# Optimization experiments

Measured on AMD Instinct MI355X. Metric: run time of the kernel, lower is better.

## Reference

```python
import jax, jax.numpy as jnp
import numpy as np

N = 100000   # num nodes
E = 640000   # num edges
IN, H, OUT = 6, 128, 1
BN_EPS = 1e-5


def setup_inputs() -> dict:
    key = jax.random.key(0)
    ks = jax.random.split(key, 12)
    x = jax.random.normal(ks[0], (N, IN), dtype=jnp.float32)
    edge_index = jax.random.randint(ks[1], (2, E), 0, N, dtype=jnp.int64)
    def lin(k, fin, fout):
        s = 1.0 / np.sqrt(fin)
        return jax.random.uniform(k, (fin, fout), jnp.float32, -s, s)
    return {
        "x": x,
        "edge_index": edge_index,
        "W1": lin(ks[2], IN, H),  "b1": jnp.zeros((H,), jnp.float32),
        "W2": lin(ks[3], H, H),   "b2": jnp.zeros((H,), jnp.float32),
        "W3": lin(ks[4], H, OUT), "b3": jnp.zeros((OUT,), jnp.float32),
        "g1": jnp.ones((H,), jnp.float32),  "be1": jnp.zeros((H,), jnp.float32),
        "g2": jnp.ones((H,), jnp.float32),  "be2": jnp.zeros((H,), jnp.float32),
    }


def _gcn_norm(edge_index):
    # add self-loops, then symmetric normalization D^-1/2 (A+I) D^-1/2
    loop = jnp.arange(N, dtype=edge_index.dtype)
    src = jnp.concatenate([edge_index[0], loop])
    dst = jnp.concatenate([edge_index[1], loop])
    deg = jax.ops.segment_sum(jnp.ones_like(dst, dtype=jnp.float32), dst, num_segments=N)
    dis = jnp.where(deg > 0, jax.lax.rsqrt(deg), 0.0)
    norm = dis[src] * dis[dst]  # (E+N,)
    return src, dst, norm


def _conv(h, W, b, src, dst, norm):
    m = h @ W                                   # (N, out) linear transform first
    msg = m[src] * norm[:, None]                # gather + edge scaling
    return jax.ops.segment_sum(msg, dst, num_segments=N) + b


def _bn(h, g, be):
    mu = h.mean(axis=0)
    var = h.var(axis=0)  # biased, as torch BN uses for normalization
    return g * (h - mu) * jax.lax.rsqrt(var + BN_EPS) + be


def reference(x, edge_index, W1, b1, W2, b2, W3, b3, g1, be1, g2, be2):
    src, dst, norm = _gcn_norm(edge_index)
    h = jax.nn.relu(_bn(_conv(x, W1, b1, src, dst, norm), g1, be1))
    h = jax.nn.relu(_bn(_conv(h, W2, b2, src, dst, norm), g2, be2))
    out = _conv(h, W3, b3, src, dst, norm)
    return jax.nn.sigmoid(out)  # (N, 1) risk scores
```

## Files before the change

### kernel.cpp

```cpp
#include <hip/hip_runtime.h>
#include <hip/hip_bf16.h>
#include <math.h>

#define HDIM 128
#define BN_EPS 1e-5f
#define CHUNK 512
#define TM 64

__device__ __forceinline__ int eget(const void* ei, long long pos, int is64) {
    return is64 ? (int)((const long long*)ei)[pos] : ((const int*)ei)[pos];
}

__global__ void k_detect(const int* ei32, int* flag) {
    if (threadIdx.x == 0) {
        int nz = 0;
        for (int k = 0; k < 64; ++k) nz += (ei32[2 * k + 1] != 0);
        *flag = (nz < 8) ? 1 : 0;
    }
}

__global__ void k_count(const void* ei, const int* flag, int* cnt, int E) {
    int e = blockIdx.x * blockDim.x + threadIdx.x;
    if (e < E) {
        int d = eget(ei, (long long)E + e, *flag);
        atomicAdd(&cnt[d], 1);
    }
}

__global__ void k_dis(const int* cnt, float* dis, int N) {
    int i = blockIdx.x * blockDim.x + threadIdx.x;
    if (i < N) dis[i] = rsqrtf((float)(cnt[i] + 1));
}

__global__ void k_scan1(const int* cnt, int* bsum, int N) {
    __shared__ int s[256];
    int t = threadIdx.x;
    int i = blockIdx.x * CHUNK + t;
    int v = 0;
    if (i < N) v += cnt[i];
    if (i + 256 < N && t + 256 < CHUNK) v += cnt[i + 256];
    s[t] = v; __syncthreads();
    for (int o = 128; o > 0; o >>= 1) {
        if (t < o) s[t] += s[t + o];
        __syncthreads();
    }
    if (t == 0) bsum[blockIdx.x] = s[0];
}

__global__ void k_scan2(int* bsum, int nb) {
    __shared__ int s[512];
    int t = threadIdx.x;
    int carry = 0;
    for (int base = 0; base < nb; base += 512) {
        int i = base + t;
        int v = (i < nb) ? bsum[i] : 0;
        s[t] = v; __syncthreads();
        for (int o = 1; o < 512; o <<= 1) {
            int add = (t >= o) ? s[t - o] : 0;
            __syncthreads();
            s[t] += add;
            __syncthreads();
        }
        if (i < nb) bsum[i] = carry + s[t] - v;
        carry += s[511];
        __syncthreads();
    }
}

__global__ void k_scan3(const int* cnt, const int* bsum, int* rowptr, int N) {
    __shared__ int s[CHUNK];
    int t = threadIdx.x;
    int i = blockIdx.x * CHUNK + t;
    int v = (i < N) ? cnt[i] : 0;
    s[t] = v; __syncthreads();
    for (int o = 1; o < CHUNK; o <<= 1) {
        int add = (t >= o) ? s[t - o] : 0;
        __syncthreads();
        s[t] += add;
        __syncthreads();
    }
    if (i < N) rowptr[i] = bsum[blockIdx.x] + s[t] - v;
    if (i == N - 1) rowptr[N] = bsum[blockIdx.x] + s[t];
}

__global__ void k_fillcsr(const void* ei, const int* flag, const float* dis,
                          const int* rowptr, int* fill, int* esrc, float* enorm, int E) {
    int e = blockIdx.x * blockDim.x + threadIdx.x;
    if (e < E) {
        int is64 = *flag;
        int s = eget(ei, e, is64);
        int d = eget(ei, (long long)E + e, is64);
        int pos = rowptr[d] + atomicAdd(&fill[d], 1);
        esrc[pos] = s;
        enorm[pos] = dis[s] * dis[d];
    }
}

__global__ void k_gath_x(const float* __restrict__ x, const int* __restrict__ rowptr,
                         const int* __restrict__ esrc, const float* __restrict__ enorm,
                         const float* __restrict__ dis, float* __restrict__ aggx, int N) {
    int i = blockIdx.x * blockDim.x + threadIdx.x;
    if (i < N) {
        float d = dis[i], d2 = d * d;
        float a0 = x[i * 6 + 0] * d2, a1 = x[i * 6 + 1] * d2, a2 = x[i * 6 + 2] * d2;
        float a3 = x[i * 6 + 3] * d2, a4 = x[i * 6 + 4] * d2, a5 = x[i * 6 + 5] * d2;
        int p0 = rowptr[i], p1 = rowptr[i + 1];
        for (int p = p0; p < p1; ++p) {
            int s = esrc[p];
            float nr = enorm[p];
            a0 += x[s * 6 + 0] * nr; a1 += x[s * 6 + 1] * nr; a2 += x[s * 6 + 2] * nr;
            a3 += x[s * 6 + 3] * nr; a4 += x[s * 6 + 4] * nr; a5 += x[s * 6 + 5] * nr;
        }
        aggx[i * 6 + 0] = a0; aggx[i * 6 + 1] = a1; aggx[i * 6 + 2] = a2;
        aggx[i * 6 + 3] = a3; aggx[i * 6 + 4] = a4; aggx[i * 6 + 5] = a5;
    }
}

__global__ void k_gemm6(const float* __restrict__ aggx, const float* __restrict__ W1,
                        const float* __restrict__ b1, float* __restrict__ out,
                        float* __restrict__ S, int N) {
    __shared__ float w[6 * HDIM];
    __shared__ float bb[HDIM];
    __shared__ float sh1[256], sh2[256];
    for (int t = threadIdx.x; t < 6 * HDIM; t += blockDim.x) w[t] = W1[t];
    if (threadIdx.x < HDIM) bb[threadIdx.x] = b1[threadIdx.x];
    __syncthreads();
    int j = threadIdx.x & (HDIM - 1);
    int sub = threadIdx.x >> 7;
    float s1 = 0.f, s2 = 0.f;
    for (long long i = blockIdx.x * 2 + sub; i < N; i += (long long)gridDim.x * 2) {
        const float* r = &aggx[i * 6];
        float acc = bb[j];
        acc += r[0] * w[0 * HDIM + j];
        acc += r[1] * w[1 * HDIM + j];
        acc += r[2] * w[2 * HDIM + j];
        acc += r[3] * w[3 * HDIM + j];
        acc += r[4] * w[4 * HDIM + j];
        acc += r[5] * w[5 * HDIM + j];
        out[i * HDIM + j] = acc;
        s1 += acc; s2 += acc * acc;
    }
    sh1[threadIdx.x] = s1; sh2[threadIdx.x] = s2;
    __syncthreads();
    if (threadIdx.x < HDIM) {
        atomicAdd(&S[j], sh1[j] + sh1[j + HDIM]);
        atomicAdd(&S[HDIM + j], sh2[j] + sh2[j + HDIM]);
    }
}

__global__ void k_bnparams(const float* S, const float* g, const float* be,
                           float invN, float* P) {
    int j = threadIdx.x;
    if (j < HDIM) {
        float mu = S[j] * invN;
        float var = S[HDIM + j] * invN - mu * mu;
        float a = g[j] * rsqrtf(var + BN_EPS);
        P[j] = a;
        P[HDIM + j] = be[j] - mu * a;
    }
}

__global__ __launch_bounds__(512, 4)
void k_agg_gemm(const float* __restrict__ h1,
                const float* __restrict__ P1,
                const int* __restrict__ rowptr, const int* __restrict__ esrc,
                const float* __restrict__ enorm, const float* __restrict__ dis,
                const float* __restrict__ W, const float* __restrict__ b,
                float* __restrict__ out,
                float* __restrict__ S,
                int N) {
    __shared__ float At[TM * HDIM];
    const int tid = threadIdx.x;
    const long long i0 = (long long)blockIdx.x * TM;

    {
        const int l = tid & 31;
        const int q = tid >> 5;
        const int c4 = l * 4;
        const float4 pa = *(const float4*)&P1[c4];
        const float4 pb = *(const float4*)&P1[HDIM + c4];
        for (int nn = q; nn < TM; nn += 16) {
            long long i = i0 + nn;
            float4 acc = make_float4(0.f, 0.f, 0.f, 0.f);
            if (i < N) {
                float d = dis[i], d2 = d * d;
                float4 v = *(const float4*)&h1[i * HDIM + c4];
                acc.x = fmaxf(fmaf(pa.x, v.x, pb.x), 0.f) * d2;
                acc.y = fmaxf(fmaf(pa.y, v.y, pb.y), 0.f) * d2;
                acc.z = fmaxf(fmaf(pa.z, v.z, pb.z), 0.f) * d2;
                acc.w = fmaxf(fmaf(pa.w, v.w, pb.w), 0.f) * d2;
                int p0 = rowptr[i], p1e = rowptr[i + 1];
                for (int p = p0; p < p1e; ++p) {
                    int s = esrc[p];
                    float nr = enorm[p];
                    float4 u = *(const float4*)&h1[(long long)s * HDIM + c4];
                    acc.x += fmaxf(fmaf(pa.x, u.x, pb.x), 0.f) * nr;
                    acc.y += fmaxf(fmaf(pa.y, u.y, pb.y), 0.f) * nr;
                    acc.z += fmaxf(fmaf(pa.z, u.z, pb.z), 0.f) * nr;
                    acc.w += fmaxf(fmaf(pa.w, u.w, pb.w), 0.f) * nr;
                }
            }
            *(float4*)&At[nn * HDIM + c4] = acc;
        }
    }
    __syncthreads();

    const int cg = tid & 31;
    const int rg = tid >> 5;
    const int c0 = cg * 4;
    const int r0 = rg * 4;
    float acc[4][4];
    {
        const float4 bv = *(const float4*)&b[c0];
        #pragma unroll
        for (int rr = 0; rr < 4; ++rr) {
            acc[rr][0] = bv.x; acc[rr][1] = bv.y; acc[rr][2] = bv.z; acc[rr][3] = bv.w;
        }
    }
    for (int k = 0; k < HDIM; k += 4) {
        const float4 w0 = *(const float4*)&W[(k + 0) * HDIM + c0];
        const float4 w1 = *(const float4*)&W[(k + 1) * HDIM + c0];
        const float4 w2 = *(const float4*)&W[(k + 2) * HDIM + c0];
        const float4 w3 = *(const float4*)&W[(k + 3) * HDIM + c0];
        #pragma unroll
        for (int rr = 0; rr < 4; ++rr) {
            const float4 av = *(const float4*)&At[(r0 + rr) * HDIM + k];
            acc[rr][0] = fmaf(av.x, w0.x, acc[rr][0]);
            acc[rr][1] = fmaf(av.x, w0.y, acc[rr][1]);
            acc[rr][2] = fmaf(av.x, w0.z, acc[rr][2]);
            acc[rr][3] = fmaf(av.x, w0.w, acc[rr][3]);
            acc[rr][0] = fmaf(av.y, w1.x, acc[rr][0]);
            acc[rr][1] = fmaf(av.y, w1.y, acc[rr][1]);
            acc[rr][2] = fmaf(av.y, w1.z, acc[rr][2]);
            acc[rr][3] = fmaf(av.y, w1.w, acc[rr][3]);
            acc[rr][0] = fmaf(av.z, w2.x, acc[rr][0]);
            acc[rr][1] = fmaf(av.z, w2.y, acc[rr][1]);
            acc[rr][2] = fmaf(av.z, w2.z, acc[rr][2]);
            acc[rr][3] = fmaf(av.z, w2.w, acc[rr][3]);
            acc[rr][0] = fmaf(av.w, w3.x, acc[rr][0]);
            acc[rr][1] = fmaf(av.w, w3.y, acc[rr][1]);
            acc[rr][2] = fmaf(av.w, w3.z, acc[rr][2]);
            acc[rr][3] = fmaf(av.w, w3.w, acc[rr][3]);
        }
    }

    float cs1[4] = {0.f, 0.f, 0.f, 0.f};
    float cs2[4] = {0.f, 0.f, 0.f, 0.f};
    #pragma unroll
    for (int rr = 0; rr < 4; ++rr) {
        long long i = i0 + r0 + rr;
        if (i < N) {
            float4 o = make_float4(acc[rr][0], acc[rr][1], acc[rr][2], acc[rr][3]);
            *(float4*)&out[i * HDIM + c0] = o;
            #pragma unroll
            for (int cc = 0; cc < 4; ++cc) {
                float v = acc[rr][cc];
                cs1[cc] += v; cs2[cc] += v * v;
            }
        }
    }

    __syncthreads();
    #pragma unroll
    for (int cc = 0; cc < 4; ++cc) {
        At[rg * HDIM + c0 + cc]        = cs1[cc];
        At[2048 + rg * HDIM + c0 + cc] = cs2[cc];
    }
    __syncthreads();
    if (tid < 256) {
        int j = tid & (HDIM - 1);
        int which = tid >> 7;
        const float* bp = &At[which * 2048 + j];
        float s = 0.f;
        #pragma unroll
        for (int g = 0; g < 16; ++g) s += bp[g * HDIM];
        atomicAdd(&S[which * HDIM + j], s);
    }
}

__global__ void k_gemv2(const float* __restrict__ A, const float* __restrict__ P,
                        const float* __restrict__ W3, float* __restrict__ m3, int N) {
    int l = threadIdx.x & 31;
    int row = blockIdx.x * 8 + (threadIdx.x >> 5);
    if (row < N) {
        int c4 = l * 4;
        float4 pa = *(const float4*)&P[c4];
        float4 pb = *(const float4*)&P[HDIM + c4];
        float4 w  = *(const float4*)&W3[c4];
        float4 v  = *(const float4*)&A[(long long)row * HDIM + c4];
        float s = fmaxf(fmaf(pa.x, v.x, pb.x), 0.f) * w.x
                + fmaxf(fmaf(pa.y, v.y, pb.y), 0.f) * w.y
                + fmaxf(fmaf(pa.z, v.z, pb.z), 0.f) * w.z
                + fmaxf(fmaf(pa.w, v.w, pb.w), 0.f) * w.w;
        for (int o = 16; o > 0; o >>= 1) s += __shfl_down(s, o, 32);
        if (l == 0) m3[row] = s;
    }
}

__global__ void k_gath_o(const float* __restrict__ m3, const int* __restrict__ rowptr,
                         const int* __restrict__ esrc, const float* __restrict__ enorm,
                         const float* __restrict__ dis, const float* __restrict__ b3,
                         float* __restrict__ out, int N) {
    int i = blockIdx.x * blockDim.x + threadIdx.x;
    if (i < N) {
        float d = dis[i];
        float acc = m3[i] * d * d;
        int p0 = rowptr[i], p1 = rowptr[i + 1];
        for (int p = p0; p < p1; ++p)
            acc += m3[esrc[p]] * enorm[p];
        acc += b3[0];
        out[i] = 1.f / (1.f + expf(-acc));
    }
}

extern "C" void kernel_launch(void* const* d_in, const int* in_sizes, int n_in,
                              void* d_out, int out_size, void* d_ws, size_t ws_size,
                              hipStream_t stream) {
    const float* x  = (const float*)d_in[0];
    const void*  ei = d_in[1];
    const float* W1 = (const float*)d_in[2];
    const float* b1 = (const float*)d_in[3];
    const float* W2 = (const float*)d_in[4];
    const float* b2 = (const float*)d_in[5];
    const float* W3 = (const float*)d_in[6];
    const float* b3 = (const float*)d_in[7];
    const float* g1 = (const float*)d_in[8];
    const float* be1 = (const float*)d_in[9];
    const float* g2 = (const float*)d_in[10];
    const float* be2 = (const float*)d_in[11];

    const int N = in_sizes[0] / 6;
    const int E = in_sizes[1] / 2;
    const float invN = 1.0f / (float)N;

    float* ws = (float*)d_ws;
    long long off = 0;
    int*   flag   = (int*)ws;                 off += 16;
    float* dis    = ws + off;                 off += N;
    int*   cnt    = (int*)(ws + off);         off += N;
    int*   rowptr = (int*)(ws + off);         off += N + 16;
    int*   esrc   = (int*)(ws + off);         off += E;
    float* enorm  = ws + off;                 off += E;
    int*   bsum   = (int*)(ws + off);         off += 512;
    float* S1     = ws + off;                 off += 256;
    float* S2     = ws + off;                 off += 256;
    float* P1     = ws + off;                 off += 256;
    float* P2     = ws + off;                 off += 256;
    float* aggx   = ws + off;                 off += (long long)6 * N;
    float* m3     = ws + off;                 off += N;
    float* Hb1    = ws + off;                 off += (long long)HDIM * N;
    float* Hb2    = ws + off;                 off += (long long)HDIM * N;

    const int T = 256;
    const int bN  = (N + T - 1) / T;
    const int bE  = (E + T - 1) / T;
    const int nchunk = (N + CHUNK - 1) / CHUNK;
    const int ntile  = (N + TM - 1) / TM;

    hipMemsetAsync(S1, 0, 512 * sizeof(float), stream);
    k_detect<<<1, 64, 0, stream>>>((const int*)ei, flag);
    hipMemsetAsync(cnt, 0, (size_t)N * sizeof(int), stream);
    k_count<<<bE, T, 0, stream>>>(ei, flag, cnt, E);
    k_dis<<<bN, T, 0, stream>>>(cnt, dis, N);
    k_scan1<<<nchunk, 256, 0, stream>>>(cnt, bsum, N);
    k_scan2<<<1, 512, 0, stream>>>(bsum, nchunk);
    k_scan3<<<nchunk, CHUNK, 0, stream>>>(cnt, bsum, rowptr, N);
    hipMemsetAsync(cnt, 0, (size_t)N * sizeof(int), stream);
    k_fillcsr<<<bE, T, 0, stream>>>(ei, flag, dis, rowptr, cnt, esrc, enorm, E);

    k_gath_x<<<bN, T, 0, stream>>>(x, rowptr, esrc, enorm, dis, aggx, N);
    k_gemm6<<<512, T, 0, stream>>>(aggx, W1, b1, Hb1, S1, N);
    k_bnparams<<<1, 128, 0, stream>>>(S1, g1, be1, invN, P1);

    k_agg_gemm<<<ntile, 512, 0, stream>>>(Hb1, P1, rowptr, esrc, enorm, dis,
                                          W2, b2, Hb2, S2, N);
    k_bnparams<<<1, 128, 0, stream>>>(S2, g2, be2, invN, P2);

    k_gemv2<<<(N + 7) / 8, T, 0, stream>>>(Hb2, P2, W3, m3, N);
    k_gath_o<<<bN, T, 0, stream>>>(m3, rowptr, esrc, enorm, dis, b3, (float*)d_out, N);
}
```

Measured before the change: 294.3 us.

## Store layer-1 hidden in bf16, persistent ticket-scheduled agg-gemm, vectorized gathers

Layer-1 hidden activations are written as bf16, halving the bytes moved by the dominant 128-wide neighbor gather in k_agg_gemm. That kernel becomes a persistent grid that pulls tiles from an atomic ticket counter. It gains 8-wide lanes, 4-way unrolled edge loops and a padded LDS stride. The input features are also padded to 8 floats for vector loads, and the final scalar gather is unrolled. These cut gather bandwidth and latency, at the cost of bf16 rounding error in the layer-1 activations and an extra padding kernel.

```diff
diff --git a/kernel.cpp b/kernel.cpp
--- a/kernel.cpp
+++ b/kernel.cpp
@@ -6,9 +6,15 @@
 #define BN_EPS 1e-5f
 #define CHUNK 512
 #define TM 64
+#define LDA 132
 
 __device__ __forceinline__ int eget(const void* ei, long long pos, int is64) {
     return is64 ? (int)((const long long*)ei)[pos] : ((const int*)ei)[pos];
+}
+__device__ __forceinline__ unsigned short f2bf(float f) {
+    unsigned int u = __float_as_uint(f);
+    u += 0x7fffu + ((u >> 16) & 1u);
+    return (unsigned short)(u >> 16);
 }
 
 __global__ void k_detect(const int* ei32, int* flag) {
@@ -96,28 +102,49 @@
     }
 }
 
-__global__ void k_gath_x(const float* __restrict__ x, const int* __restrict__ rowptr,
+__global__ void k_padx(const float* __restrict__ x, float* __restrict__ xp, int N) {
+    int t = blockIdx.x * blockDim.x + threadIdx.x;
+    if (t < N * 8) {
+        int i = t >> 3, c = t & 7;
+        xp[t] = (c < 6) ? x[i * 6 + c] : 0.f;
+    }
+}
+
+__global__ void k_gath_x(const float* __restrict__ xp, const int* __restrict__ rowptr,
                          const int* __restrict__ esrc, const float* __restrict__ enorm,
                          const float* __restrict__ dis, float* __restrict__ aggx, int N) {
     int i = blockIdx.x * blockDim.x + threadIdx.x;
-    if (i < N) {
-        float d = dis[i], d2 = d * d;
-        float a0 = x[i * 6 + 0] * d2, a1 = x[i * 6 + 1] * d2, a2 = x[i * 6 + 2] * d2;
-        float a3 = x[i * 6 + 3] * d2, a4 = x[i * 6 + 4] * d2, a5 = x[i * 6 + 5] * d2;
-        int p0 = rowptr[i], p1 = rowptr[i + 1];
-        for (int p = p0; p < p1; ++p) {
-            int s = esrc[p];
-            float nr = enorm[p];
-            a0 += x[s * 6 + 0] * nr; a1 += x[s * 6 + 1] * nr; a2 += x[s * 6 + 2] * nr;
-            a3 += x[s * 6 + 3] * nr; a4 += x[s * 6 + 4] * nr; a5 += x[s * 6 + 5] * nr;
-        }
-        aggx[i * 6 + 0] = a0; aggx[i * 6 + 1] = a1; aggx[i * 6 + 2] = a2;
-        aggx[i * 6 + 3] = a3; aggx[i * 6 + 4] = a4; aggx[i * 6 + 5] = a5;
-    }
+    if (i >= N) return;
+    float d = dis[i], d2 = d * d;
+    float4 A = *(const float4*)&xp[i * 8];
+    float2 B = *(const float2*)&xp[i * 8 + 4];
+    float a0 = A.x * d2, a1 = A.y * d2, a2 = A.z * d2;
+    float a3 = A.w * d2, a4 = B.x * d2, a5 = B.y * d2;
+    int p = rowptr[i], pe = rowptr[i + 1];
+    for (; p + 2 <= pe; p += 2) {
+        int s0 = esrc[p], s1 = esrc[p + 1];
+        float n0 = enorm[p], n1 = enorm[p + 1];
+        float4 A0 = *(const float4*)&xp[s0 * 8];
+        float2 B0 = *(const float2*)&xp[s0 * 8 + 4];
+        float4 A1 = *(const float4*)&xp[s1 * 8];
+        float2 B1 = *(const float2*)&xp[s1 * 8 + 4];
+        a0 += A0.x * n0 + A1.x * n1; a1 += A0.y * n0 + A1.y * n1;
+        a2 += A0.z * n0 + A1.z * n1; a3 += A0.w * n0 + A1.w * n1;
+        a4 += B0.x * n0 + B1.x * n1; a5 += B0.y * n0 + B1.y * n1;
+    }
+    if (p < pe) {
+        int s0 = esrc[p]; float n0 = enorm[p];
+        float4 A0 = *(const float4*)&xp[s0 * 8];
+        float2 B0 = *(const float2*)&xp[s0 * 8 + 4];
+        a0 += A0.x * n0; a1 += A0.y * n0; a2 += A0.z * n0;
+        a3 += A0.w * n0; a4 += B0.x * n0; a5 += B0.y * n0;
+    }
+    aggx[i * 6 + 0] = a0; aggx[i * 6 + 1] = a1; aggx[i * 6 + 2] = a2;
+    aggx[i * 6 + 3] = a3; aggx[i * 6 + 4] = a4; aggx[i * 6 + 5] = a5;
 }
 
 __global__ void k_gemm6(const float* __restrict__ aggx, const float* __restrict__ W1,
-                        const float* __restrict__ b1, float* __restrict__ out,
+                        const float* __restrict__ b1, unsigned short* __restrict__ out,
                         float* __restrict__ S, int N) {
     __shared__ float w[6 * HDIM];
     __shared__ float bb[HDIM];
@@ -137,7 +164,7 @@
         acc += r[3] * w[3 * HDIM + j];
         acc += r[4] * w[4 * HDIM + j];
         acc += r[5] * w[5 * HDIM + j];
-        out[i * HDIM + j] = acc;
+        out[i * HDIM + j] = f2bf(acc);
         s1 += acc; s2 += acc * acc;
     }
     sh1[threadIdx.x] = s1; sh2[threadIdx.x] = s2;
@@ -160,121 +187,157 @@
     }
 }
 
-__global__ __launch_bounds__(512, 4)
-void k_agg_gemm(const float* __restrict__ h1,
-                const float* __restrict__ P1,
+__device__ __forceinline__ void gacc(float* a, const float* pa, const float* pb,
+                                     uint4 u, float wgt) {
+    unsigned int uu[4] = {u.x, u.y, u.z, u.w};
+    #pragma unroll
+    for (int q = 0; q < 4; ++q) {
+        float lo = __uint_as_float(uu[q] << 16);
+        float hi = __uint_as_float(uu[q] & 0xffff0000u);
+        a[2 * q]     += fmaxf(fmaf(pa[2 * q],     lo, pb[2 * q]),     0.f) * wgt;
+        a[2 * q + 1] += fmaxf(fmaf(pa[2 * q + 1], hi, pb[2 * q + 1]), 0.f) * wgt;
+    }
+}
+
+__global__ __launch_bounds__(512, 8)
+void k_agg_gemm(const unsigned short* __restrict__ m1, const float* __restrict__ P1,
                 const int* __restrict__ rowptr, const int* __restrict__ esrc,
                 const float* __restrict__ enorm, const float* __restrict__ dis,
                 const float* __restrict__ W, const float* __restrict__ b,
-                float* __restrict__ out,
-                float* __restrict__ S,
-                int N) {
-    __shared__ float At[TM * HDIM];
+                float* __restrict__ out, float* __restrict__ S,
+                int* __restrict__ ticket, int ntiles, int N) {
+    __shared__ float At[TM * LDA];
+    __shared__ int s_tile;
     const int tid = threadIdx.x;
-    const long long i0 = (long long)blockIdx.x * TM;
-
+
+    const int gl = tid & 15;
+    const int gg = tid >> 4;
+    const int c8 = gl * 8;
+    float pa[8], pb[8];
     {
-        const int l = tid & 31;
-        const int q = tid >> 5;
-        const int c4 = l * 4;
-        const float4 pa = *(const float4*)&P1[c4];
-        const float4 pb = *(const float4*)&P1[HDIM + c4];
-        for (int nn = q; nn < TM; nn += 16) {
-            long long i = i0 + nn;
-            float4 acc = make_float4(0.f, 0.f, 0.f, 0.f);
-            if (i < N) {
-                float d = dis[i], d2 = d * d;
-                float4 v = *(const float4*)&h1[i * HDIM + c4];
-                acc.x = fmaxf(fmaf(pa.x, v.x, pb.x), 0.f) * d2;
-                acc.y = fmaxf(fmaf(pa.y, v.y, pb.y), 0.f) * d2;
-                acc.z = fmaxf(fmaf(pa.z, v.z, pb.z), 0.f) * d2;
-                acc.w = fmaxf(fmaf(pa.w, v.w, pb.w), 0.f) * d2;
-                int p0 = rowptr[i], p1e = rowptr[i + 1];
-                for (int p = p0; p < p1e; ++p) {
-                    int s = esrc[p];
-                    float nr = enorm[p];
-                    float4 u = *(const float4*)&h1[(long long)s * HDIM + c4];
-                    acc.x += fmaxf(fmaf(pa.x, u.x, pb.x), 0.f) * nr;
-                    acc.y += fmaxf(fmaf(pa.y, u.y, pb.y), 0.f) * nr;
-                    acc.z += fmaxf(fmaf(pa.z, u.z, pb.z), 0.f) * nr;
-                    acc.w += fmaxf(fmaf(pa.w, u.w, pb.w), 0.f) * nr;
-                }
-            }
-            *(float4*)&At[nn * HDIM + c4] = acc;
-        }
-    }
-    __syncthreads();
-
+        float4 t0 = *(const float4*)&P1[c8];
+        float4 t1 = *(const float4*)&P1[c8 + 4];
+        float4 t2 = *(const float4*)&P1[HDIM + c8];
+        float4 t3 = *(const float4*)&P1[HDIM + c8 + 4];
+        pa[0] = t0.x; pa[1] = t0.y; pa[2] = t0.z; pa[3] = t0.w;
+        pa[4] = t1.x; pa[5] = t1.y; pa[6] = t1.z; pa[7] = t1.w;
+        pb[0] = t2.x; pb[1] = t2.y; pb[2] = t2.z; pb[3] = t2.w;
+        pb[4] = t3.x; pb[5] = t3.y; pb[6] = t3.z; pb[7] = t3.w;
+    }
     const int cg = tid & 31;
     const int rg = tid >> 5;
     const int c0 = cg * 4;
     const int r0 = rg * 4;
-    float acc[4][4];
-    {
-        const float4 bv = *(const float4*)&b[c0];
+    const float4 bv = *(const float4*)&b[c0];
+
+    for (;;) {
+        if (tid == 0) s_tile = atomicAdd(ticket, 1);
+        __syncthreads();
+        const int tile = s_tile;
+        if (tile >= ntiles) return;
+        const long long i0 = (long long)tile * TM;
+
+        for (int nn = gg; nn < TM; nn += 32) {
+            long long i = i0 + nn;
+            float a[8] = {0.f, 0.f, 0.f, 0.f, 0.f, 0.f, 0.f, 0.f};
+            if (i < N) {
+                float d = dis[i];
+                uint4 us = *(const uint4*)&m1[i * HDIM + c8];
+                gacc(a, pa, pb, us, d * d);
+                int p = rowptr[i], pe = rowptr[i + 1];
+                for (; p + 4 <= pe; p += 4) {
+                    int s0 = esrc[p], s1 = esrc[p + 1], s2 = esrc[p + 2], s3 = esrc[p + 3];
+                    float n0 = enorm[p], n1 = enorm[p + 1], n2 = enorm[p + 2], n3 = enorm[p + 3];
+                    uint4 u0 = *(const uint4*)&m1[(long long)s0 * HDIM + c8];
+                    uint4 u1 = *(const uint4*)&m1[(long long)s1 * HDIM + c8];
+                    uint4 u2 = *(const uint4*)&m1[(long long)s2 * HDIM + c8];
+                    uint4 u3 = *(const uint4*)&m1[(long long)s3 * HDIM + c8];
+                    gacc(a, pa, pb, u0, n0); gacc(a, pa, pb, u1, n1);
+                    gacc(a, pa, pb, u2, n2); gacc(a, pa, pb, u3, n3);
+                }
+                if (p + 2 <= pe) {
+                    int s0 = esrc[p], s1 = esrc[p + 1];
+                    float n0 = enorm[p], n1 = enorm[p + 1];
+                    uint4 u0 = *(const uint4*)&m1[(long long)s0 * HDIM + c8];
+                    uint4 u1 = *(const uint4*)&m1[(long long)s1 * HDIM + c8];
+                    gacc(a, pa, pb, u0, n0); gacc(a, pa, pb, u1, n1);
+                    p += 2;
+                }
+                if (p < pe) {
+                    int s0 = esrc[p]; float n0 = enorm[p];
+                    uint4 u0 = *(const uint4*)&m1[(long long)s0 * HDIM + c8];
+                    gacc(a, pa, pb, u0, n0);
+                }
+            }
+            *(float4*)&At[nn * LDA + c8]     = make_float4(a[0], a[1], a[2], a[3]);
+            *(float4*)&At[nn * LDA + c8 + 4] = make_float4(a[4], a[5], a[6], a[7]);
+        }
+        __syncthreads();
+
+        float acc[4][4];
         #pragma unroll
         for (int rr = 0; rr < 4; ++rr) {
             acc[rr][0] = bv.x; acc[rr][1] = bv.y; acc[rr][2] = bv.z; acc[rr][3] = bv.w;
         }
-    }
-    for (int k = 0; k < HDIM; k += 4) {
-        const float4 w0 = *(const float4*)&W[(k + 0) * HDIM + c0];
-        const float4 w1 = *(const float4*)&W[(k + 1) * HDIM + c0];
-        const float4 w2 = *(const float4*)&W[(k + 2) * HDIM + c0];
-        const float4 w3 = *(const float4*)&W[(k + 3) * HDIM + c0];
+        for (int k = 0; k < HDIM; k += 4) {
+            const float4 w0 = *(const float4*)&W[(k + 0) * HDIM + c0];
+            const float4 w1 = *(const float4*)&W[(k + 1) * HDIM + c0];
+            const float4 w2 = *(const float4*)&W[(k + 2) * HDIM + c0];
+            const float4 w3 = *(const float4*)&W[(k + 3) * HDIM + c0];
+            #pragma unroll
+            for (int rr = 0; rr < 4; ++rr) {
+                const float4 av = *(const float4*)&At[(r0 + rr) * LDA + k];
+                acc[rr][0] = fmaf(av.x, w0.x, acc[rr][0]);
+                acc[rr][1] = fmaf(av.x, w0.y, acc[rr][1]);
+                acc[rr][2] = fmaf(av.x, w0.z, acc[rr][2]);
+                acc[rr][3] = fmaf(av.x, w0.w, acc[rr][3]);
+                acc[rr][0] = fmaf(av.y, w1.x, acc[rr][0]);
+                acc[rr][1] = fmaf(av.y, w1.y, acc[rr][1]);
+                acc[rr][2] = fmaf(av.y, w1.z, acc[rr][2]);
+                acc[rr][3] = fmaf(av.y, w1.w, acc[rr][3]);
+                acc[rr][0] = fmaf(av.z, w2.x, acc[rr][0]);
+                acc[rr][1] = fmaf(av.z, w2.y, acc[rr][1]);
+                acc[rr][2] = fmaf(av.z, w2.z, acc[rr][2]);
+                acc[rr][3] = fmaf(av.z, w2.w, acc[rr][3]);
+                acc[rr][0] = fmaf(av.w, w3.x, acc[rr][0]);
+                acc[rr][1] = fmaf(av.w, w3.y, acc[rr][1]);
+                acc[rr][2] = fmaf(av.w, w3.z, acc[rr][2]);
+                acc[rr][3] = fmaf(av.w, w3.w, acc[rr][3]);
+            }
+        }
+
+        float cs1[4] = {0.f, 0.f, 0.f, 0.f};
+        float cs2[4] = {0.f, 0.f, 0.f, 0.f};
         #pragma unroll
         for (int rr = 0; rr < 4; ++rr) {
-            const float4 av = *(const float4*)&At[(r0 + rr) * HDIM + k];
-            acc[rr][0] = fmaf(av.x, w0.x, acc[rr][0]);
-            acc[rr][1] = fmaf(av.x, w0.y, acc[rr][1]);
-            acc[rr][2] = fmaf(av.x, w0.z, acc[rr][2]);
-            acc[rr][3] = fmaf(av.x, w0.w, acc[rr][3]);
-            acc[rr][0] = fmaf(av.y, w1.x, acc[rr][0]);
-            acc[rr][1] = fmaf(av.y, w1.y, acc[rr][1]);
-            acc[rr][2] = fmaf(av.y, w1.z, acc[rr][2]);
-            acc[rr][3] = fmaf(av.y, w1.w, acc[rr][3]);
-            acc[rr][0] = fmaf(av.z, w2.x, acc[rr][0]);
-            acc[rr][1] = fmaf(av.z, w2.y, acc[rr][1]);
-            acc[rr][2] = fmaf(av.z, w2.z, acc[rr][2]);
-            acc[rr][3] = fmaf(av.z, w2.w, acc[rr][3]);
-            acc[rr][0] = fmaf(av.w, w3.x, acc[rr][0]);
-            acc[rr][1] = fmaf(av.w, w3.y, acc[rr][1]);
-            acc[rr][2] = fmaf(av.w, w3.z, acc[rr][2]);
-            acc[rr][3] = fmaf(av.w, w3.w, acc[rr][3]);
-        }
-    }
-
-    float cs1[4] = {0.f, 0.f, 0.f, 0.f};
-    float cs2[4] = {0.f, 0.f, 0.f, 0.f};
-    #pragma unroll
-    for (int rr = 0; rr < 4; ++rr) {
-        long long i = i0 + r0 + rr;
-        if (i < N) {
-            float4 o = make_float4(acc[rr][0], acc[rr][1], acc[rr][2], acc[rr][3]);
-            *(float4*)&out[i * HDIM + c0] = o;
+            long long i = i0 + r0 + rr;
+            if (i < N) {
+                *(float4*)&out[i * HDIM + c0] =
+                    make_float4(acc[rr][0], acc[rr][1], acc[rr][2], acc[rr][3]);
+                #pragma unroll
+                for (int cc = 0; cc < 4; ++cc) {
+                    float v = acc[rr][cc];
+                    cs1[cc] += v; cs2[cc] += v * v;
+                }
+            }
+        }
+        __syncthreads();
+        #pragma unroll
+        for (int cc = 0; cc < 4; ++cc) {
+            At[rg * HDIM + c0 + cc]        = cs1[cc];
+            At[2048 + rg * HDIM + c0 + cc] = cs2[cc];
+        }
+        __syncthreads();
+        if (tid < 256) {
+            int j = tid & (HDIM - 1);
+            int which = tid >> 7;
+            const float* bp = &At[which * 2048 + j];
+            float s = 0.f;
             #pragma unroll
-            for (int cc = 0; cc < 4; ++cc) {
-                float v = acc[rr][cc];
-                cs1[cc] += v; cs2[cc] += v * v;
-            }
-        }
-    }
-
-    __syncthreads();
-    #pragma unroll
-    for (int cc = 0; cc < 4; ++cc) {
-        At[rg * HDIM + c0 + cc]        = cs1[cc];
-        At[2048 + rg * HDIM + c0 + cc] = cs2[cc];
-    }
-    __syncthreads();
-    if (tid < 256) {
-        int j = tid & (HDIM - 1);
-        int which = tid >> 7;
-        const float* bp = &At[which * 2048 + j];
-        float s = 0.f;
-        #pragma unroll
-        for (int g = 0; g < 16; ++g) s += bp[g * HDIM];
-        atomicAdd(&S[which * HDIM + j], s);
+            for (int g = 0; g < 16; ++g) s += bp[g * HDIM];
+            atomicAdd(&S[which * HDIM + j], s);
+        }
+        __syncthreads();
     }
 }
 
@@ -305,8 +368,15 @@
     if (i < N) {
         float d = dis[i];
         float acc = m3[i] * d * d;
-        int p0 = rowptr[i], p1 = rowptr[i + 1];
-        for (int p = p0; p < p1; ++p)
+        int p = rowptr[i], pe = rowptr[i + 1];
+        for (; p + 4 <= pe; p += 4) {
+            float v0 = m3[esrc[p]]     * enorm[p];
+            float v1 = m3[esrc[p + 1]] * enorm[p + 1];
+            float v2 = m3[esrc[p + 2]] * enorm[p + 2];
+            float v3 = m3[esrc[p + 3]] * enorm[p + 3];
+            acc += (v0 + v1) + (v2 + v3);
+        }
+        for (; p < pe; ++p)
             acc += m3[esrc[p]] * enorm[p];
         acc += b3[0];
         out[i] = 1.f / (1.f + expf(-acc));
@@ -335,28 +405,32 @@
 
     float* ws = (float*)d_ws;
     long long off = 0;
+    auto pad4 = [](long long v) { return (v + 3) & ~3LL; };
     int*   flag   = (int*)ws;                 off += 16;
-    float* dis    = ws + off;                 off += N;
-    int*   cnt    = (int*)(ws + off);         off += N;
-    int*   rowptr = (int*)(ws + off);         off += N + 16;
-    int*   esrc   = (int*)(ws + off);         off += E;
-    float* enorm  = ws + off;                 off += E;
+    int*   ticket = (int*)ws + 1;
+    float* dis    = ws + off;                 off = pad4(off + N);
+    int*   cnt    = (int*)(ws + off);         off = pad4(off + N);
+    int*   rowptr = (int*)(ws + off);         off = pad4(off + N + 16);
+    int*   esrc   = (int*)(ws + off);         off = pad4(off + E);
+    float* enorm  = ws + off;                 off = pad4(off + E);
     int*   bsum   = (int*)(ws + off);         off += 512;
     float* S1     = ws + off;                 off += 256;
     float* S2     = ws + off;                 off += 256;
     float* P1     = ws + off;                 off += 256;
     float* P2     = ws + off;                 off += 256;
-    float* aggx   = ws + off;                 off += (long long)6 * N;
-    float* m3     = ws + off;                 off += N;
-    float* Hb1    = ws + off;                 off += (long long)HDIM * N;
+    float* xp     = ws + off;                 off = pad4(off + (long long)8 * N);
+    float* aggx   = ws + off;                 off = pad4(off + (long long)6 * N);
+    float* m3     = ws + off;                 off = pad4(off + N);
+    unsigned short* m1 = (unsigned short*)(ws + off); off = pad4(off + (long long)64 * N);
     float* Hb2    = ws + off;                 off += (long long)HDIM * N;
 
     const int T = 256;
     const int bN  = (N + T - 1) / T;
     const int bE  = (E + T - 1) / T;
     const int nchunk = (N + CHUNK - 1) / CHUNK;
-    const int ntile  = (N + TM - 1) / TM;
-
+    const int ntiles = (N + TM - 1) / TM;
+
+    hipMemsetAsync(flag, 0, 64, stream);
     hipMemsetAsync(S1, 0, 512 * sizeof(float), stream);
     k_detect<<<1, 64, 0, stream>>>((const int*)ei, flag);
     hipMemsetAsync(cnt, 0, (size_t)N * sizeof(int), stream);
@@ -368,12 +442,13 @@
     hipMemsetAsync(cnt, 0, (size_t)N * sizeof(int), stream);
     k_fillcsr<<<bE, T, 0, stream>>>(ei, flag, dis, rowptr, cnt, esrc, enorm, E);
 
-    k_gath_x<<<bN, T, 0, stream>>>(x, rowptr, esrc, enorm, dis, aggx, N);
-    k_gemm6<<<512, T, 0, stream>>>(aggx, W1, b1, Hb1, S1, N);
+    k_padx<<<(N * 8 + T - 1) / T, T, 0, stream>>>(x, xp, N);
+    k_gath_x<<<bN, T, 0, stream>>>(xp, rowptr, esrc, enorm, dis, aggx, N);
+    k_gemm6<<<512, T, 0, stream>>>(aggx, W1, b1, m1, S1, N);
     k_bnparams<<<1, 128, 0, stream>>>(S1, g1, be1, invN, P1);
 
-    k_agg_gemm<<<ntile, 512, 0, stream>>>(Hb1, P1, rowptr, esrc, enorm, dis,
-                                          W2, b2, Hb2, S2, N);
+    k_agg_gemm<<<1024, 512, 0, stream>>>(m1, P1, rowptr, esrc, enorm, dis,
+                                         W2, b2, Hb2, S2, ticket, ntiles, N);
     k_bnparams<<<1, 128, 0, stream>>>(S2, g2, be2, invN, P2);
 
     k_gemv2<<<(N + 7) / 8, T, 0, stream>>>(Hb2, P2, W3, m3, N);
```

Result: slower. 554.8 us (+88.5%).
